# Kernel tuning notes

Hardware: AMD Instinct MI355X
Metric: run time of the kernel (lower is better)

## Reference

```python
import jax, jax.numpy as jnp
import numpy as np

# MORRConfig_20um_MQ (all-pass MRR) constants used by mrr_roundtrip_phase_to_tr(intensity=True)
A = 0.987   # attenuation_factor a
R = 0.99    # coupling_factor r
KS, STRIDE, PAD = 3, 1, 1
IN_C, OUT_C, MB = 32, 64, 8


def _unfold(x, ks, pad, stride):
    # torch.nn.functional.unfold: output channel order is (C, kh, kw), C slowest
    B, C, H, W = x.shape
    xp = jnp.pad(x, ((0, 0), (0, 0), (pad, pad), (pad, pad)))
    Ho = (H + 2 * pad - ks) // stride + 1
    Wo = (W + 2 * pad - ks) // stride + 1
    cols = jnp.stack(
        [xp[:, :, i:i + stride * Ho:stride, j:j + stride * Wo:stride]
         for i in range(ks) for j in range(ks)],
        axis=2,
    )  # [B, C, ks*ks, Ho, Wo]
    return cols.reshape(B, C * ks * ks, Ho * Wo), Ho, Wo


def _mrr_tr(phase):
    # all-pass MRR intensity transmission vs roundtrip phase detuning
    c = jnp.cos(phase)
    return (A * A - 2.0 * A * R * c + R * R) / (1.0 - 2.0 * A * R * c + (A * R) ** 2)


def setup_inputs() -> dict:
    key = jax.random.key(0)
    k1, k2, k3 = jax.random.split(key, 3)
    B, H, W = 8, 64, 64
    wic = IN_C * KS * KS           # 288, divisible by miniblock -> no zero pad
    q = wic // MB                  # grid_dim_x = 36
    p = OUT_C // MB                # grid_dim_y = 8
    x = jax.random.normal(k1, (B, IN_C, H, W), jnp.float32)
    weight = jax.random.normal(k2, (p, q, MB), jnp.float32)
    morr_output_scale = jax.random.normal(k3, (max(1, q // 2) + 1,), jnp.float32)
    return {"x": x, "weight": weight, "morr_output_scale": morr_output_scale}


def reference(x, weight, morr_output_scale):
    B = x.shape[0]
    p, q, k = weight.shape
    w = jnp.abs(weight)                                  # w_bit=16 -> build_weight() = |W|
    cols, Ho, Wo = _unfold(x, KS, PAD, STRIDE)           # [B, wic, L]
    xf = cols.transpose(0, 2, 1).reshape(-1, q, k)       # [N, q, k], N = B*Ho*Wo
    xf = xf * xf                                         # intensity modulation x^2
    # block-circulant matvec via rFFT (circular convolution per (p, q) block)
    Xf = jnp.fft.rfft(xf, n=k, axis=-1)                  # [N, q, kf]
    Wf = jnp.fft.rfft(w, n=k, axis=-1)                   # [p, q, kf]
    phase = jnp.fft.irfft(Xf[:, None, :, :] * Wf[None, :, :, :], n=k, axis=-1)  # [N, p, q, k]
    tr = _mrr_tr(phase)                                  # MORR nonlinear transfer
    # differential-rail output scale (even grid_dim_x branch)
    s = morr_output_scale
    if q % 2 == 0:
        scale = jnp.concatenate([s[:-1], -s[:-1]])
    else:
        scale = jnp.concatenate([s[:-1], s[-1:], -s[:-1]])
    out = jnp.einsum('npqk,q->npk', tr, scale).reshape(-1, p * k)[:, :OUT_C]
    return out.reshape(B, Ho, Wo, OUT_C).transpose(0, 3, 1, 2)  # [B, OUT_C, Ho, Wo]
```

## Files before the change

kernel.cpp:

```cpp
#include <hip/hip_runtime.h>
#include <math.h>


__global__ __launch_bounds__(512, 4)
void morr_kernel(const float* __restrict__ xg, const float* __restrict__ wg,
                 const float* __restrict__ sg, float* __restrict__ out) {
    __shared__ __align__(16) float lds_x[32 * 10 * 24];
    __shared__ __align__(16) float lds_w[8 * 36 * 8];
    __shared__ float lds_nds[36];

    constexpr double Ad = 0.987, Rd = 0.99;
    constexpr float K2 = (float)(2.0 * Ad * Rd);
    constexpr float C2 = (float)(1.0 + (Ad * Rd) * (Ad * Rd));
    constexpr float D  = (float)((1.0 - Ad * Ad) * (1.0 - Rd * Rd));

    const int tid = threadIdx.x;
    const int b  = blockIdx.z;
    const int tr = blockIdx.y;
    const int tc = blockIdx.x;
    const int gr0 = tr * 8, gc0 = tc * 16;

    for (int i = tid; i < 32 * 10 * 18; i += 512) {
        int c = i / 180, rem = i - c * 180;
        int r = rem / 18, cl = rem - r * 18;
        int gr = gr0 - 1 + r, gc = gc0 - 1 + cl;
        float v = 0.f;
        if ((unsigned)gr < 64u && (unsigned)gc < 64u)
            v = xg[((b * 32 + c) * 64 + gr) * 64 + gc];
        lds_x[c * 240 + r * 24 + cl] = v * v;
    }
    for (int i = tid; i < 2304; i += 512) lds_w[i] = fabsf(wg[i]);
    if (tid < 36) {
        float sv = (tid < 18) ? sg[tid] : -sg[tid - 18];
        lds_nds[tid] = -D * sv;
    }
    __syncthreads();

    const int px   = tid & 127;
    const int pgrp = tid >> 7;
    const int row  = px >> 4;
    const int col  = px & 15;
    const int tb   = row * 24 + col;

    float acc[2][8];
#pragma unroll
    for (int pp = 0; pp < 2; ++pp)
#pragma unroll
        for (int t = 0; t < 8; ++t) acc[pp][t] = 0.f;

    float xq[8];
    for (int cb = 0; cb < 4; ++cb) {
        const int xb = tb + cb * 1920;
        const int wb = (pgrp * 2) * 288 + cb * 72;
        const int nb = cb * 9;
#pragma unroll
        for (int u = 0; u < 72; ++u) {
            const int cc = u / 9;
            const int rr = (u % 9) / 3;
            const int ww = u % 3;
            xq[u & 7] = lds_x[xb + cc * 240 + rr * 24 + ww];
            if ((u & 7) == 7) {
                const int qq = u >> 3;
                const float nds = lds_nds[nb + qq];
#pragma unroll
                for (int pp = 0; pp < 2; ++pp) {
                    const float4 wa = *reinterpret_cast<const float4*>(
                        &lds_w[wb + pp * 288 + qq * 8]);
                    const float4 wc = *reinterpret_cast<const float4*>(
                        &lds_w[wb + pp * 288 + qq * 8 + 4]);
                    const float wv[8] = {wa.x, wa.y, wa.z, wa.w,
                                         wc.x, wc.y, wc.z, wc.w};
#pragma unroll
                    for (int t = 0; t < 8; ++t) {
                        float ph = xq[0] * wv[t];
#pragma unroll
                        for (int s = 1; s < 8; ++s)
                            ph = fmaf(xq[s], wv[(t - s) & 7], ph);
                        float cv  = __cosf(ph);
                        float den = fmaf(-K2, cv, C2);
                        float inv = __builtin_amdgcn_rcpf(den);
                        acc[pp][t] = fmaf(nds, inv, acc[pp][t]);
                    }
                }
            }
        }
    }

    const int gr = gr0 + row, gc = gc0 + col;
    const int pb = pgrp * 2;
#pragma unroll
    for (int pp = 0; pp < 2; ++pp)
#pragma unroll
        for (int t = 0; t < 8; ++t) {
            const int oc = (pb + pp) * 8 + t;
            out[(b * 64 + oc) * 4096 + gr * 64 + gc] = acc[pp][t];
        }
}

extern "C" void kernel_launch(void* const* d_in, const int* in_sizes, int n_in,
                              void* d_out, int out_size, void* d_ws, size_t ws_size,
                              hipStream_t stream) {
    const float* x = (const float*)d_in[0];
    const float* w = (const float*)d_in[1];
    const float* s = (const float*)d_in[2];
    float* out = (float*)d_out;
    dim3 grid(4, 8, 8);
    dim3 block(512);
    hipLaunchKernelGGL(morr_kernel, grid, block, 0, stream, x, w, s, out);
}
```

Baseline: 112.5 us.

## Use 1024-thread blocks with one output group per thread and native cosine

Doubles the block to 1024 threads so each thread computes a single 8-channel output group instead of two, which halves per-thread accumulators and x reuse. The weights are prescaled by 1/(2π) when loaded so the hardware v_cos instruction (which takes its input in revolutions) can be called directly, avoiding the range-reduction multiply inside __cosf. Each x value is now loaded from LDS by twice as many threads, and the larger block may limit how many blocks fit per CU.

```diff
diff --git a/kernel.cpp b/kernel.cpp
--- a/kernel.cpp
+++ b/kernel.cpp
@@ -2,7 +2,7 @@
 #include <math.h>
 
 
-__global__ __launch_bounds__(512, 4)
+__global__ __launch_bounds__(1024, 4)
 void morr_kernel(const float* __restrict__ xg, const float* __restrict__ wg,
                  const float* __restrict__ sg, float* __restrict__ out) {
     __shared__ __align__(16) float lds_x[32 * 10 * 24];
@@ -13,6 +13,7 @@
     constexpr float K2 = (float)(2.0 * Ad * Rd);
     constexpr float C2 = (float)(1.0 + (Ad * Rd) * (Ad * Rd));
     constexpr float D  = (float)((1.0 - Ad * Ad) * (1.0 - Rd * Rd));
+    constexpr float INV2PI = 0.15915494309189535f;
 
     const int tid = threadIdx.x;
     const int b  = blockIdx.z;
@@ -20,7 +21,7 @@
     const int tc = blockIdx.x;
     const int gr0 = tr * 8, gc0 = tc * 16;
 
-    for (int i = tid; i < 32 * 10 * 18; i += 512) {
+    for (int i = tid; i < 32 * 10 * 18; i += 1024) {
         int c = i / 180, rem = i - c * 180;
         int r = rem / 18, cl = rem - r * 18;
         int gr = gr0 - 1 + r, gc = gc0 - 1 + cl;
@@ -29,29 +30,27 @@
             v = xg[((b * 32 + c) * 64 + gr) * 64 + gc];
         lds_x[c * 240 + r * 24 + cl] = v * v;
     }
-    for (int i = tid; i < 2304; i += 512) lds_w[i] = fabsf(wg[i]);
+    for (int i = tid; i < 2304; i += 1024) lds_w[i] = fabsf(wg[i]) * INV2PI;
     if (tid < 36) {
         float sv = (tid < 18) ? sg[tid] : -sg[tid - 18];
         lds_nds[tid] = -D * sv;
     }
     __syncthreads();
 
-    const int px   = tid & 127;
-    const int pgrp = tid >> 7;
-    const int row  = px >> 4;
-    const int col  = px & 15;
-    const int tb   = row * 24 + col;
+    const int px  = tid & 127;
+    const int p   = tid >> 7;
+    const int row = px >> 4;
+    const int col = px & 15;
+    const int tb  = row * 24 + col;
 
-    float acc[2][8];
+    float acc[8];
 #pragma unroll
-    for (int pp = 0; pp < 2; ++pp)
-#pragma unroll
-        for (int t = 0; t < 8; ++t) acc[pp][t] = 0.f;
+    for (int t = 0; t < 8; ++t) acc[t] = 0.f;
 
     float xq[8];
     for (int cb = 0; cb < 4; ++cb) {
         const int xb = tb + cb * 1920;
-        const int wb = (pgrp * 2) * 288 + cb * 72;
+        const int wb = p * 288 + cb * 72;
         const int nb = cb * 9;
 #pragma unroll
         for (int u = 0; u < 72; ++u) {
@@ -62,39 +61,33 @@
             if ((u & 7) == 7) {
                 const int qq = u >> 3;
                 const float nds = lds_nds[nb + qq];
+                const float4 wa = *reinterpret_cast<const float4*>(
+                    &lds_w[wb + qq * 8]);
+                const float4 wc = *reinterpret_cast<const float4*>(
+                    &lds_w[wb + qq * 8 + 4]);
+                const float wv[8] = {wa.x, wa.y, wa.z, wa.w,
+                                     wc.x, wc.y, wc.z, wc.w};
 #pragma unroll
-                for (int pp = 0; pp < 2; ++pp) {
-                    const float4 wa = *reinterpret_cast<const float4*>(
-                        &lds_w[wb + pp * 288 + qq * 8]);
-                    const float4 wc = *reinterpret_cast<const float4*>(
-                        &lds_w[wb + pp * 288 + qq * 8 + 4]);
-                    const float wv[8] = {wa.x, wa.y, wa.z, wa.w,
-                                         wc.x, wc.y, wc.z, wc.w};
+                for (int t = 0; t < 8; ++t) {
+                    float ph = xq[0] * wv[t];
 #pragma unroll
-                    for (int t = 0; t < 8; ++t) {
-                        float ph = xq[0] * wv[t];
-#pragma unroll
-                        for (int s = 1; s < 8; ++s)
-                            ph = fmaf(xq[s], wv[(t - s) & 7], ph);
-                        float cv  = __cosf(ph);
-                        float den = fmaf(-K2, cv, C2);
-                        float inv = __builtin_amdgcn_rcpf(den);
-                        acc[pp][t] = fmaf(nds, inv, acc[pp][t]);
-                    }
+                    for (int s = 1; s < 8; ++s)
+                        ph = fmaf(xq[s], wv[(t - s) & 7], ph);
+                    float cv  = __builtin_amdgcn_cosf(ph);
+                    float den = fmaf(-K2, cv, C2);
+                    float inv = __builtin_amdgcn_rcpf(den);
+                    acc[t] = fmaf(nds, inv, acc[t]);
                 }
             }
         }
     }
 
     const int gr = gr0 + row, gc = gc0 + col;
-    const int pb = pgrp * 2;
 #pragma unroll
-    for (int pp = 0; pp < 2; ++pp)
-#pragma unroll
-        for (int t = 0; t < 8; ++t) {
-            const int oc = (pb + pp) * 8 + t;
-            out[(b * 64 + oc) * 4096 + gr * 64 + gc] = acc[pp][t];
-        }
+    for (int t = 0; t < 8; ++t) {
+        const int oc = p * 8 + t;
+        out[(b * 64 + oc) * 4096 + gr * 64 + gc] = acc[t];
+    }
 }
 
 extern "C" void kernel_launch(void* const* d_in, const int* in_sizes, int n_in,
@@ -105,6 +98,6 @@
     const float* s = (const float*)d_in[2];
     float* out = (float*)d_out;
     dim3 grid(4, 8, 8);
-    dim3 block(512);
+    dim3 block(1024);
     hipLaunchKernelGGL(morr_kernel, grid, block, 0, stream, x, w, s, out);
 }
```

Result: faster. 90.53 us (-19.6%).
